# Kernel tuning notes

Measured on AMD Instinct MI355X. Metric: run time of the kernel, lower is better.

Reference implementation:

```python
import jax, jax.numpy as jnp
import numpy as np

D = 2048      # input_dim
E = 64        # num_experts
TOPK = 8
N = 16384     # tokens


def setup_inputs() -> dict:
    key = jax.random.key(0)
    k_x, k_w1, k_b1, k_w2, k_b2 = jax.random.split(key, 5)
    s1 = 1.0 / np.sqrt(D)
    return {
        "x": jax.random.normal(k_x, (N, D), dtype=jnp.float32),
        "W1": jax.random.uniform(k_w1, (D, D), minval=-s1, maxval=s1, dtype=jnp.float32),
        "b1": jax.random.uniform(k_b1, (D,), minval=-s1, maxval=s1, dtype=jnp.float32),
        "W2": jax.random.uniform(k_w2, (D, E), minval=-s1, maxval=s1, dtype=jnp.float32),
        "b2": jax.random.uniform(k_b2, (E,), minval=-s1, maxval=s1, dtype=jnp.float32),
    }


def reference(x, W1, b1, W2, b2):
    # gate MLP: Linear -> GELU (exact, erf-based as torch nn.GELU default) -> Linear
    h = jax.nn.gelu(x @ W1 + b1, approximate=False)
    logits = h @ W2 + b2                              # [N, E]
    # eval mode: no noise added
    top_vals, top_idx = jax.lax.top_k(logits, TOPK)   # [N, K]
    top_w = jax.nn.softmax(top_vals, axis=-1)         # softmax over selected logits
    rows = jnp.arange(logits.shape[0])[:, None]       # [N, 1]
    routing_weights = jnp.zeros_like(logits).at[rows, top_idx].set(top_w)
    # load balance loss
    probs = jax.nn.softmax(logits, axis=-1)
    freq = (routing_weights > 0).astype(logits.dtype).mean(axis=0)   # [E]
    avg_prob = probs.mean(axis=0)                                    # [E]
    load_balance_loss = E * jnp.sum(freq * avg_prob)
    return routing_weights, top_idx, load_balance_loss
```

## Files before the change

### kernel.cpp

```cpp
#include <hip/hip_runtime.h>
#include <math.h>
#include <stdint.h>

#define N_TOK 16384
#define DIM   2048
#define NEXP  64
#define TOPK  8

#define BM 128
#define BN 128
#define BKE 32

typedef _Float16 half8 __attribute__((ext_vector_type(8)));
typedef _Float16 half4 __attribute__((ext_vector_type(4)));
typedef float    f32x4 __attribute__((ext_vector_type(4)));

#define GLOBAL_AS __attribute__((address_space(1)))
#define LDS_AS    __attribute__((address_space(3)))

#define LO_SCALE     4096.0f
#define INV_LO_SCALE (1.0f / 4096.0f)

__device__ inline uint32_t pack_split(float v) {
    _Float16 hi = (_Float16)v;
    float r = (v - (float)hi) * LO_SCALE;
    _Float16 lo = (_Float16)r;
    return (uint32_t)__builtin_bit_cast(uint16_t, hi) |
           ((uint32_t)__builtin_bit_cast(uint16_t, lo) << 16);
}

__device__ inline _Float16 split_hi(float v) { return (_Float16)v; }
__device__ inline _Float16 split_lo(float v) {
    _Float16 hi = (_Float16)v;
    return (_Float16)((v - (float)hi) * LO_SCALE);
}

union U4H8 { uint32_t u[4]; half8 h; };

__device__ inline void load_frag(const uint32_t* base, int row, int quad,
                                 half8& hi, half8& lo) {
    const int sw = row & 7;
    const uint4 q0 = *(const uint4*)(base + row * 32 + (((quad * 2)     ^ sw) << 2));
    const uint4 q1 = *(const uint4*)(base + row * 32 + (((quad * 2 + 1) ^ sw) << 2));
    uint32_t u[8] = {q0.x, q0.y, q0.z, q0.w, q1.x, q1.y, q1.z, q1.w};
    U4H8 H, L;
    #pragma unroll
    for (int j = 0; j < 4; j++) {
        H.u[j] = (u[2 * j] & 0xffffu) | (u[2 * j + 1] << 16);
        L.u[j] = (u[2 * j] >> 16)     | (u[2 * j + 1] & 0xffff0000u);
    }
    hi = H.h; lo = L.h;
}

__device__ inline void load_frag2(const _Float16* base, int row, int quad,
                                  half8& hi, half8& lo) {
    const int sw = row & 7;
    hi = *(const half8*)(base + row * 64 + ((quad       ^ sw) << 3));
    lo = *(const half8*)(base + row * 64 + (((quad + 4) ^ sw) << 3));
}

__global__ __launch_bounds__(256) void convert_x_split(
    const float* __restrict__ x, _Float16* __restrict__ xhi,
    _Float16* __restrict__ xlo)
{
    size_t i = ((size_t)blockIdx.x * 256 + threadIdx.x) * 4;
    float4 v = *(const float4*)(x + i);
    half4 h, l;
    h.x = split_hi(v.x); l.x = split_lo(v.x);
    h.y = split_hi(v.y); l.y = split_lo(v.y);
    h.z = split_hi(v.z); l.z = split_lo(v.z);
    h.w = split_hi(v.w); l.w = split_lo(v.w);
    *(half4*)(xhi + i) = h;
    *(half4*)(xlo + i) = l;
}

__global__ __launch_bounds__(256) void convert_w1t_split(
    const float* __restrict__ W1, _Float16* __restrict__ w1hi,
    _Float16* __restrict__ w1lo)
{
    __shared__ float s[32][33];
    const int k0 = blockIdx.y * 32, n0 = blockIdx.x * 32;
    const int tr = threadIdx.x & 31, tc = threadIdx.x >> 5;
    #pragma unroll
    for (int r = 0; r < 4; r++) {
        int row = tc + r * 8;
        s[row][tr] = W1[(size_t)(k0 + row) * DIM + n0 + tr];
    }
    __syncthreads();
    #pragma unroll
    for (int r = 0; r < 4; r++) {
        int row = tc + r * 8;
        float v = s[tr][row];
        w1hi[(size_t)(n0 + row) * DIM + k0 + tr] = split_hi(v);
        w1lo[(size_t)(n0 + row) * DIM + k0 + tr] = split_lo(v);
    }
}

__global__ __launch_bounds__(256) void convert_w2t(const float* __restrict__ W2,
                                                   uint32_t* __restrict__ W2Tp) {
    int i = blockIdx.x * 256 + threadIdx.x;
    int e = i >> 11, n = i & 2047;
    W2Tp[i] = pack_split(W2[(size_t)n * NEXP + e]);
}

__global__ __launch_bounds__(256) void convert_x_inplace(float* __restrict__ x) {
    size_t i = ((size_t)blockIdx.x * 256 + threadIdx.x) * 4;
    float4 v = *(const float4*)(x + i);
    uint4 p;
    p.x = pack_split(v.x); p.y = pack_split(v.y);
    p.z = pack_split(v.z); p.w = pack_split(v.w);
    *(uint4*)(x + i) = p;
}

__global__ __launch_bounds__(256) void convert_w1t_packed(
    const float* __restrict__ W1, uint32_t* __restrict__ W1Tp)
{
    __shared__ float s[32][33];
    const int k0 = blockIdx.y * 32, n0 = blockIdx.x * 32;
    const int tr = threadIdx.x & 31, tc = threadIdx.x >> 5;
    #pragma unroll
    for (int r = 0; r < 4; r++) {
        int row = tc + r * 8;
        s[row][tr] = W1[(size_t)(k0 + row) * DIM + n0 + tr];
    }
    __syncthreads();
    #pragma unroll
    for (int r = 0; r < 4; r++) {
        int row = tc + r * 8;
        W1Tp[(size_t)(n0 + row) * DIM + k0 + tr] = pack_split(s[tr][row]);
    }
}

__global__ __launch_bounds__(256, 2) void gemm_fused_v2(
    const _Float16* __restrict__ xhi, const _Float16* __restrict__ xlo,
    const _Float16* __restrict__ w1hi, const _Float16* __restrict__ w1lo,
    const float* __restrict__ b1, const uint32_t* __restrict__ W2Tp,
    float* __restrict__ Lp)
{
    __shared__ uint32_t smem[16384];
    _Float16* As = (_Float16*)smem;
    _Float16* Bs = (_Float16*)(smem + 4096);

    const int t    = threadIdx.x;
    const int wid  = t >> 6;
    const int lane = t & 63;
    const int quad = lane >> 4;
    const int l16  = lane & 15;

    const int lin = blockIdx.x;
    const int grp = lin >> 7;
    const int rem = lin & 127;
    const int m0 = (grp * 8 + (rem & 7)) * BM;
    const int n0 = (rem >> 3) * BN;

    const _Float16* gA[4];
    const _Float16* gB[4];
    #pragma unroll
    for (int r = 0; r < 4; r++) {
        int s_lin = r * 256 + t;
        int row = s_lin >> 3;
        int c   = (s_lin & 7) ^ (row & 7);
        gA[r] = (c < 4) ? xhi  + (size_t)(m0 + row) * DIM + c * 8
                        : xlo  + (size_t)(m0 + row) * DIM + (c - 4) * 8;
        gB[r] = (c < 4) ? w1hi + (size_t)(n0 + row) * DIM + c * 8
                        : w1lo + (size_t)(n0 + row) * DIM + (c - 4) * 8;
    }

    f32x4 am[4][4], ac[4][4];
    #pragma unroll
    for (int i = 0; i < 4; i++)
        #pragma unroll
        for (int j = 0; j < 4; j++) { am[i][j] = (f32x4)0.0f; ac[i][j] = (f32x4)0.0f; }

    const int wm = (wid & 1) * 64;
    const int wn = (wid >> 1) * 64;

    for (int k0 = 0; k0 < DIM; k0 += BKE) {
        #pragma unroll
        for (int r = 0; r < 4; r++) {
            const int wslot = (r * 256 + wid * 64) << 2;
            __builtin_amdgcn_global_load_lds((const GLOBAL_AS uint32_t*)gA[r],
                                             (LDS_AS uint32_t*)(smem + wslot), 16, 0, 0);
            __builtin_amdgcn_global_load_lds((const GLOBAL_AS uint32_t*)gB[r],
                                             (LDS_AS uint32_t*)(smem + 4096 + wslot), 16, 0, 0);
            gA[r] += BKE; gB[r] += BKE;
        }
        __syncthreads();

        half8 ah[4], al[4], bh[4], bl[4];
        #pragma unroll
        for (int mt = 0; mt < 4; mt++)
            load_frag2(As, wm + mt * 16 + l16, quad, ah[mt], al[mt]);
        #pragma unroll
        for (int nt = 0; nt < 4; nt++)
            load_frag2(Bs, wn + nt * 16 + l16, quad, bh[nt], bl[nt]);

        #pragma unroll
        for (int mt = 0; mt < 4; mt++)
            #pragma unroll
            for (int nt = 0; nt < 4; nt++) {
                am[mt][nt] = __builtin_amdgcn_mfma_f32_16x16x32_f16(ah[mt], bh[nt], am[mt][nt], 0, 0, 0);
                ac[mt][nt] = __builtin_amdgcn_mfma_f32_16x16x32_f16(ah[mt], bl[nt], ac[mt][nt], 0, 0, 0);
                ac[mt][nt] = __builtin_amdgcn_mfma_f32_16x16x32_f16(al[mt], bh[nt], ac[mt][nt], 0, 0, 0);
            }
        __syncthreads();
    }

    uint32_t* Hs = smem;
    #pragma unroll
    for (int mt = 0; mt < 4; mt++)
        #pragma unroll
        for (int nt = 0; nt < 4; nt++) {
            const int coln = wn + nt * 16 + l16;
            const float b1v = b1[n0 + coln];
            #pragma unroll
            for (int r = 0; r < 4; r++) {
                float h = am[mt][nt][r] + ac[mt][nt][r] * INV_LO_SCALE + b1v;
                h = 0.5f * h * (1.0f + erff(h * 0.70710678118654752440f));
                const int rowm = wm + mt * 16 + quad * 4 + r;
                const int word = rowm * 128 + ((((coln >> 2) ^ (rowm & 7)) << 2) | (coln & 3));
                Hs[word] = pack_split(h);
            }
        }
    __syncthreads();

    f32x4 a2m[2][4], a2c[2][4];
    #pragma unroll
    for (int i = 0; i < 2; i++)
        #pragma unroll
        for (int j = 0; j < 4; j++) { a2m[i][j] = (f32x4)0.0f; a2c[i][j] = (f32x4)0.0f; }

    #pragma unroll
    for (int ks = 0; ks < 4; ks++) {
        half8 a2h[2], a2l[2];
        #pragma unroll
        for (int mt2 = 0; mt2 < 2; mt2++) {
            const int row = wid * 32 + mt2 * 16 + l16;
            const int sw  = row & 7;
            const int cb  = ks * 8 + quad * 2;
            const uint4 q0 = *(const uint4*)(Hs + row * 128 + ((cb ^ sw) << 2));
            const uint4 q1 = *(const uint4*)(Hs + row * 128 + (((cb + 1) ^ sw) << 2));
            uint32_t u[8] = {q0.x, q0.y, q0.z, q0.w, q1.x, q1.y, q1.z, q1.w};
            U4H8 H, L;
            #pragma unroll
            for (int j = 0; j < 4; j++) {
                H.u[j] = (u[2 * j] & 0xffffu) | (u[2 * j + 1] << 16);
                L.u[j] = (u[2 * j] >> 16)     | (u[2 * j + 1] & 0xffff0000u);
            }
            a2h[mt2] = H.h; a2l[mt2] = L.h;
        }
        #pragma unroll
        for (int et = 0; et < 4; et++) {
            const int e = et * 16 + l16;
            const uint32_t* wp = W2Tp + (size_t)e * DIM + n0 + ks * 32 + quad * 8;
            const uint4 q0 = *(const uint4*)wp;
            const uint4 q1 = *(const uint4*)(wp + 4);
            uint32_t u[8] = {q0.x, q0.y, q0.z, q0.w, q1.x, q1.y, q1.z, q1.w};
            U4H8 H, L;
            #pragma unroll
            for (int j = 0; j < 4; j++) {
                H.u[j] = (u[2 * j] & 0xffffu) | (u[2 * j + 1] << 16);
                L.u[j] = (u[2 * j] >> 16)     | (u[2 * j + 1] & 0xffff0000u);
            }
            #pragma unroll
            for (int mt2 = 0; mt2 < 2; mt2++) {
                a2m[mt2][et] = __builtin_amdgcn_mfma_f32_16x16x32_f16(a2h[mt2], H.h, a2m[mt2][et], 0, 0, 0);
                a2c[mt2][et] = __builtin_amdgcn_mfma_f32_16x16x32_f16(a2h[mt2], L.h, a2c[mt2][et], 0, 0, 0);
                a2c[mt2][et] = __builtin_amdgcn_mfma_f32_16x16x32_f16(a2l[mt2], H.h, a2c[mt2][et], 0, 0, 0);
            }
        }
    }

    #pragma unroll
    for (int mt2 = 0; mt2 < 2; mt2++)
        #pragma unroll
        for (int et = 0; et < 4; et++)
            #pragma unroll
            for (int r = 0; r < 4; r++) {
                const float lg = a2m[mt2][et][r] + a2c[mt2][et][r] * INV_LO_SCALE;
                const int rowm = m0 + wid * 32 + mt2 * 16 + quad * 4 + r;
                const int e = et * 16 + l16;
                atomicAdd(&Lp[(size_t)rowm * NEXP + e], lg);
            }
}

__global__ __launch_bounds__(256, 2) void gemm_fused(
    const uint32_t* __restrict__ xp, const uint32_t* __restrict__ W1Tp,
    const float* __restrict__ b1, const uint32_t* __restrict__ W2Tp,
    float* __restrict__ Lp)
{
    __shared__ uint32_t smem[16384];
    uint32_t* Ap = smem;
    uint32_t* Bp = smem + 4096;

    const int t    = threadIdx.x;
    const int wid  = t >> 6;
    const int lane = t & 63;
    const int quad = lane >> 4;
    const int l16  = lane & 15;

    const int lin = blockIdx.x;
    const int grp = lin >> 7;
    const int rem = lin & 127;
    const int m0 = (grp * 8 + (rem & 7)) * BM;
    const int n0 = (rem >> 3) * BN;

    const uint32_t* gA[4];
    const uint32_t* gB[4];
    #pragma unroll
    for (int r = 0; r < 4; r++) {
        int s = r * 256 + t;
        int row = s >> 3;
        int c   = s & 7;
        int co  = (c ^ (row & 7)) << 2;
        gA[r] = xp   + (size_t)(m0 + row) * DIM + co;
        gB[r] = W1Tp + (size_t)(n0 + row) * DIM + co;
    }

    f32x4 am[4][4], ac[4][4];
    #pragma unroll
    for (int i = 0; i < 4; i++)
        #pragma unroll
        for (int j = 0; j < 4; j++) { am[i][j] = (f32x4)0.0f; ac[i][j] = (f32x4)0.0f; }

    const int wm = (wid & 1) * 64;
    const int wn = (wid >> 1) * 64;

    for (int k0 = 0; k0 < DIM; k0 += BKE) {
        #pragma unroll
        for (int r = 0; r < 4; r++) {
            const int wslot = (r * 256 + wid * 64) << 2;
            __builtin_amdgcn_global_load_lds((const GLOBAL_AS uint32_t*)gA[r],
                                             (LDS_AS uint32_t*)(Ap + wslot), 16, 0, 0);
            __builtin_amdgcn_global_load_lds((const GLOBAL_AS uint32_t*)gB[r],
                                             (LDS_AS uint32_t*)(Bp + wslot), 16, 0, 0);
            gA[r] += BKE; gB[r] += BKE;
        }
        __syncthreads();

        half8 ah[4], al[4], bh[4], bl[4];
        #pragma unroll
        for (int mt = 0; mt < 4; mt++)
            load_frag(Ap, wm + mt * 16 + l16, quad, ah[mt], al[mt]);
        #pragma unroll
        for (int nt = 0; nt < 4; nt++)
            load_frag(Bp, wn + nt * 16 + l16, quad, bh[nt], bl[nt]);

        #pragma unroll
        for (int mt = 0; mt < 4; mt++)
            #pragma unroll
            for (int nt = 0; nt < 4; nt++) {
                am[mt][nt] = __builtin_amdgcn_mfma_f32_16x16x32_f16(ah[mt], bh[nt], am[mt][nt], 0, 0, 0);
                ac[mt][nt] = __builtin_amdgcn_mfma_f32_16x16x32_f16(ah[mt], bl[nt], ac[mt][nt], 0, 0, 0);
                ac[mt][nt] = __builtin_amdgcn_mfma_f32_16x16x32_f16(al[mt], bh[nt], ac[mt][nt], 0, 0, 0);
            }
        __syncthreads();
    }

    uint32_t* Hs = smem;
    #pragma unroll
    for (int mt = 0; mt < 4; mt++)
        #pragma unroll
        for (int nt = 0; nt < 4; nt++) {
            const int coln = wn + nt * 16 + l16;
            const float b1v = b1[n0 + coln];
            #pragma unroll
            for (int r = 0; r < 4; r++) {
                float h = am[mt][nt][r] + ac[mt][nt][r] * INV_LO_SCALE + b1v;
                h = 0.5f * h * (1.0f + erff(h * 0.70710678118654752440f));
                const int rowm = wm + mt * 16 + quad * 4 + r;
                const int word = rowm * 128 + ((((coln >> 2) ^ (rowm & 7)) << 2) | (coln & 3));
                Hs[word] = pack_split(h);
            }
        }
    __syncthreads();

    f32x4 a2m[2][4], a2c[2][4];
    #pragma unroll
    for (int i = 0; i < 2; i++)
        #pragma unroll
        for (int j = 0; j < 4; j++) { a2m[i][j] = (f32x4)0.0f; a2c[i][j] = (f32x4)0.0f; }

    #pragma unroll
    for (int ks = 0; ks < 4; ks++) {
        half8 a2h[2], a2l[2];
        #pragma unroll
        for (int mt2 = 0; mt2 < 2; mt2++) {
            const int row = wid * 32 + mt2 * 16 + l16;
            const int sw  = row & 7;
            const int cb  = ks * 8 + quad * 2;
            const uint4 q0 = *(const uint4*)(Hs + row * 128 + ((cb ^ sw) << 2));
            const uint4 q1 = *(const uint4*)(Hs + row * 128 + (((cb + 1) ^ sw) << 2));
            uint32_t u[8] = {q0.x, q0.y, q0.z, q0.w, q1.x, q1.y, q1.z, q1.w};
            U4H8 H, L;
            #pragma unroll
            for (int j = 0; j < 4; j++) {
                H.u[j] = (u[2 * j] & 0xffffu) | (u[2 * j + 1] << 16);
                L.u[j] = (u[2 * j] >> 16)     | (u[2 * j + 1] & 0xffff0000u);
            }
            a2h[mt2] = H.h; a2l[mt2] = L.h;
        }
        #pragma unroll
        for (int et = 0; et < 4; et++) {
            const int e = et * 16 + l16;
            const uint32_t* wp = W2Tp + (size_t)e * DIM + n0 + ks * 32 + quad * 8;
            const uint4 q0 = *(const uint4*)wp;
            const uint4 q1 = *(const uint4*)(wp + 4);
            uint32_t u[8] = {q0.x, q0.y, q0.z, q0.w, q1.x, q1.y, q1.z, q1.w};
            U4H8 H, L;
            #pragma unroll
            for (int j = 0; j < 4; j++) {
                H.u[j] = (u[2 * j] & 0xffffu) | (u[2 * j + 1] << 16);
                L.u[j] = (u[2 * j] >> 16)     | (u[2 * j + 1] & 0xffff0000u);
            }
            #pragma unroll
            for (int mt2 = 0; mt2 < 2; mt2++) {
                a2m[mt2][et] = __builtin_amdgcn_mfma_f32_16x16x32_f16(a2h[mt2], H.h, a2m[mt2][et], 0, 0, 0);
                a2c[mt2][et] = __builtin_amdgcn_mfma_f32_16x16x32_f16(a2h[mt2], L.h, a2c[mt2][et], 0, 0, 0);
                a2c[mt2][et] = __builtin_amdgcn_mfma_f32_16x16x32_f16(a2l[mt2], H.h, a2c[mt2][et], 0, 0, 0);
            }
        }
    }

    #pragma unroll
    for (int mt2 = 0; mt2 < 2; mt2++)
        #pragma unroll
        for (int et = 0; et < 4; et++)
            #pragma unroll
            for (int r = 0; r < 4; r++) {
                const float lg = a2m[mt2][et][r] + a2c[mt2][et][r] * INV_LO_SCALE;
                const int rowm = m0 + wid * 32 + mt2 * 16 + quad * 4 + r;
                const int e = et * 16 + l16;
                atomicAdd(&Lp[(size_t)rowm * NEXP + e], lg);
            }
}

__global__ __launch_bounds__(256) void router_topk_v2(
    const float* __restrict__ Lp, const float* __restrict__ b2,
    float* __restrict__ out_rw, float* __restrict__ out_idx,
    float* __restrict__ gP, float* __restrict__ gI)
{
    __shared__ float sP[NEXP];
    __shared__ float sI[NEXP];
    const int t = threadIdx.x;
    if (t < NEXP) { sP[t] = 0.f; sI[t] = 0.f; }
    __syncthreads();

    const int lane = t & 63;
    const int wv   = t >> 6;
    const float b2v = b2[lane];

    float accP = 0.f, accSel = 0.f;

    for (int i = 0; i < 16; i++) {
        const int tok = blockIdx.x * 64 + i * 4 + wv;
        float logit = Lp[(size_t)tok * NEXP + lane] + b2v;

        float mx = logit;
        #pragma unroll
        for (int off = 32; off >= 1; off >>= 1) mx = fmaxf(mx, __shfl_xor(mx, off));
        float p = expf(logit - mx);
        float ps = p;
        #pragma unroll
        for (int off = 32; off >= 1; off >>= 1) ps += __shfl_xor(ps, off);
        accP += p / ps;

        float cur = logit;
        float tv[TOPK]; int tix[TOPK];
        for (int k = 0; k < TOPK; k++) {
            float v = cur; int idx = lane;
            #pragma unroll
            for (int off = 32; off >= 1; off >>= 1) {
                float ov = __shfl_xor(v, off);
                int   oi = __shfl_xor(idx, off);
                if (ov > v || (ov == v && oi < idx)) { v = ov; idx = oi; }
            }
            tv[k] = v; tix[k] = idx;
            if (lane == idx) cur = -INFINITY;
        }

        float ev[TOPK], s = 0.f;
        #pragma unroll
        for (int k = 0; k < TOPK; k++) { ev[k] = expf(tv[k] - tv[0]); s += ev[k]; }
        float w = 0.f;
        #pragma unroll
        for (int k = 0; k < TOPK; k++)
            if (tix[k] == lane) { w = ev[k] / s; accSel += 1.f; }

        out_rw[(size_t)tok * NEXP + lane] = w;
        if (lane < TOPK) out_idx[(size_t)tok * TOPK + lane] = (float)tix[lane];
    }

    atomicAdd(&sP[lane], accP);
    atomicAdd(&sI[lane], accSel);
    __syncthreads();
    if (t < NEXP) { atomicAdd(&gP[t], sP[t]); atomicAdd(&gI[t], sI[t]); }
}

__global__ void loss_kernel(const float* __restrict__ gP,
                            const float* __restrict__ gI,
                            float* __restrict__ out_loss)
{
    const int lane = threadIdx.x;
    const float inv = 1.0f / (float)N_TOK;
    float v = (gI[lane] * inv) * (gP[lane] * inv);
    #pragma unroll
    for (int off = 32; off >= 1; off >>= 1) v += __shfl_xor(v, off);
    if (lane == 0) out_loss[0] = (float)NEXP * v;
}

extern "C" void kernel_launch(void* const* d_in, const int* in_sizes, int n_in,
                              void* d_out, int out_size, void* d_ws, size_t ws_size,
                              hipStream_t stream) {
    const float* x  = (const float*)d_in[0];
    const float* W1 = (const float*)d_in[1];
    const float* b1 = (const float*)d_in[2];
    const float* W2 = (const float*)d_in[3];
    const float* b2 = (const float*)d_in[4];

    float* out_rw   = (float*)d_out;
    float* out_idx  = out_rw + (size_t)N_TOK * NEXP;
    float* out_loss = out_idx + (size_t)N_TOK * TOPK;

    const size_t SZ_X   = (size_t)N_TOK * DIM * 2;
    const size_t SZ_W1  = (size_t)DIM * DIM * 2;
    const size_t OFF_XHI   = 0;
    const size_t OFF_XLO   = OFF_XHI + SZ_X;
    const size_t OFF_W1HI  = OFF_XLO + SZ_X;
    const size_t OFF_W1LO  = OFF_W1HI + SZ_W1;
    const size_t OFF_W2T   = OFF_W1LO + SZ_W1;
    const size_t OFF_LP    = OFF_W2T + (size_t)DIM * NEXP * 4;
    const size_t OFF_G     = OFF_LP + (size_t)N_TOK * NEXP * 4;
    const size_t needed_v2 = OFF_G + 2 * NEXP * 4;

    const size_t P_W1T = 0;
    const size_t P_W2T = (size_t)16 << 20;
    const size_t P_LP  = (size_t)17 << 20;
    const size_t P_G   = P_LP + (size_t)N_TOK * NEXP * 4;
    const size_t needed_p = P_G + 2 * NEXP * 4;

    if (ws_size >= needed_v2) {
        _Float16* xhi  = (_Float16*)((char*)d_ws + OFF_XHI);
        _Float16* xlo  = (_Float16*)((char*)d_ws + OFF_XLO);
        _Float16* w1hi = (_Float16*)((char*)d_ws + OFF_W1HI);
        _Float16* w1lo = (_Float16*)((char*)d_ws + OFF_W1LO);
        uint32_t* W2Tp = (uint32_t*)((char*)d_ws + OFF_W2T);
        float* Lp = (float*)((char*)d_ws + OFF_LP);
        float* gP = (float*)((char*)d_ws + OFF_G);
        float* gI = gP + NEXP;

        (void)hipMemsetAsync((char*)d_ws + OFF_LP, 0,
                             (size_t)N_TOK * NEXP * 4 + 2 * NEXP * 4, stream);
        convert_x_split  <<<(N_TOK * DIM) / (256 * 4), 256, 0, stream>>>(x, xhi, xlo);
        convert_w1t_split<<<dim3(DIM / 32, DIM / 32), 256, 0, stream>>>(W1, w1hi, w1lo);
        convert_w2t      <<<(NEXP * DIM) / 256, 256, 0, stream>>>(W2, W2Tp);
        gemm_fused_v2<<<(N_TOK / BM) * (DIM / BN), 256, 0, stream>>>(
            xhi, xlo, w1hi, w1lo, b1, W2Tp, Lp);
        router_topk_v2<<<N_TOK / 64, 256, 0, stream>>>(Lp, b2, out_rw, out_idx, gP, gI);
        loss_kernel<<<1, 64, 0, stream>>>(gP, gI, out_loss);
    } else if (ws_size >= needed_p) {
        uint32_t* W1Tp = (uint32_t*)((char*)d_ws + P_W1T);
        uint32_t* W2Tp = (uint32_t*)((char*)d_ws + P_W2T);
        float* Lp = (float*)((char*)d_ws + P_LP);
        float* gP = (float*)((char*)d_ws + P_G);
        float* gI = gP + NEXP;

        (void)hipMemsetAsync((char*)d_ws + P_LP, 0,
                             (size_t)N_TOK * NEXP * 4 + 2 * NEXP * 4, stream);
        convert_x_inplace<<<(N_TOK * DIM) / (256 * 4), 256, 0, stream>>>((float*)d_in[0]);
        convert_w1t_packed<<<dim3(DIM / 32, DIM / 32), 256, 0, stream>>>(W1, W1Tp);
        convert_w2t<<<(NEXP * DIM) / 256, 256, 0, stream>>>(W2, W2Tp);
        gemm_fused<<<(N_TOK / BM) * (DIM / BN), 256, 0, stream>>>(
            (const uint32_t*)d_in[0], W1Tp, b1, W2Tp, Lp);
        router_topk_v2<<<N_TOK / 64, 256, 0, stream>>>(Lp, b2, out_rw, out_idx, gP, gI);
        loss_kernel<<<1, 64, 0, stream>>>(gP, gI, out_loss);
    }
}
```

Measured before the change: 771.7 us.

## Double-buffer LDS tiles in fused GEMM and widen x split conversion

```diff
diff --git a/kernel.cpp b/kernel.cpp
--- a/kernel.cpp
+++ b/kernel.cpp
@@ -63,15 +63,15 @@
     const float* __restrict__ x, _Float16* __restrict__ xhi,
     _Float16* __restrict__ xlo)
 {
-    size_t i = ((size_t)blockIdx.x * 256 + threadIdx.x) * 4;
-    float4 v = *(const float4*)(x + i);
-    half4 h, l;
-    h.x = split_hi(v.x); l.x = split_lo(v.x);
-    h.y = split_hi(v.y); l.y = split_lo(v.y);
-    h.z = split_hi(v.z); l.z = split_lo(v.z);
-    h.w = split_hi(v.w); l.w = split_lo(v.w);
-    *(half4*)(xhi + i) = h;
-    *(half4*)(xlo + i) = l;
+    size_t i = ((size_t)blockIdx.x * 256 + threadIdx.x) * 8;
+    float4 v0 = *(const float4*)(x + i);
+    float4 v1 = *(const float4*)(x + i + 4);
+    const float vv[8] = {v0.x, v0.y, v0.z, v0.w, v1.x, v1.y, v1.z, v1.w};
+    half8 h, l;
+    #pragma unroll
+    for (int j = 0; j < 8; j++) { h[j] = split_hi(vv[j]); l[j] = split_lo(vv[j]); }
+    *(half8*)(xhi + i) = h;
+    *(half8*)(xlo + i) = l;
 }
 
 __global__ __launch_bounds__(256) void convert_w1t_split(
@@ -131,6 +131,47 @@
     }
 }
 
+
+#define KSTEP(ASrc_, BSrc_, ASt_, BSt_, DOSTAGE_)                               \
+    {                                                                           \
+        if (DOSTAGE_) {                                                         \
+            _Pragma("unroll")                                                   \
+            for (int r = 0; r < 4; r++) {                                       \
+                const int wslot = (r * 256 + wid * 64) << 2;                    \
+                __builtin_amdgcn_global_load_lds(                               \
+                    (const GLOBAL_AS uint32_t*)gA[r],                           \
+                    (LDS_AS uint32_t*)((ASt_) + wslot), 16, 0, 0);              \
+                __builtin_amdgcn_global_load_lds(                               \
+                    (const GLOBAL_AS uint32_t*)gB[r],                           \
+                    (LDS_AS uint32_t*)((BSt_) + wslot), 16, 0, 0);              \
+                gA[r] += BKE; gB[r] += BKE;                                     \
+            }                                                                   \
+        }                                                                       \
+        half8 ah[4], al[4], bh[4], bl[4];                                       \
+        _Pragma("unroll")                                                       \
+        for (int mt = 0; mt < 4; mt++)                                          \
+            load_frag2((const _Float16*)(ASrc_), wm + mt * 16 + l16, quad,      \
+                       ah[mt], al[mt]);                                         \
+        _Pragma("unroll")                                                       \
+        for (int nt = 0; nt < 4; nt++)                                          \
+            load_frag2((const _Float16*)(BSrc_), wn + nt * 16 + l16, quad,      \
+                       bh[nt], bl[nt]);                                         \
+        __builtin_amdgcn_s_setprio(1);                                          \
+        _Pragma("unroll")                                                       \
+        for (int mt = 0; mt < 4; mt++)                                          \
+            _Pragma("unroll")                                                   \
+            for (int nt = 0; nt < 4; nt++) {                                    \
+                am[mt][nt] = __builtin_amdgcn_mfma_f32_16x16x32_f16(            \
+                    ah[mt], bh[nt], am[mt][nt], 0, 0, 0);                       \
+                ac[mt][nt] = __builtin_amdgcn_mfma_f32_16x16x32_f16(            \
+                    ah[mt], bl[nt], ac[mt][nt], 0, 0, 0);                       \
+                ac[mt][nt] = __builtin_amdgcn_mfma_f32_16x16x32_f16(            \
+                    al[mt], bh[nt], ac[mt][nt], 0, 0, 0);                       \
+            }                                                                   \
+        __builtin_amdgcn_s_setprio(0);                                          \
+        __syncthreads();                                                        \
+    }
+
 __global__ __launch_bounds__(256, 2) void gemm_fused_v2(
     const _Float16* __restrict__ xhi, const _Float16* __restrict__ xlo,
     const _Float16* __restrict__ w1hi, const _Float16* __restrict__ w1lo,
@@ -138,8 +179,10 @@
     float* __restrict__ Lp)
 {
     __shared__ uint32_t smem[16384];
-    _Float16* As = (_Float16*)smem;
-    _Float16* Bs = (_Float16*)(smem + 4096);
+    uint32_t* A0 = smem;
+    uint32_t* B0 = smem + 4096;
+    uint32_t* A1 = smem + 8192;
+    uint32_t* B1 = smem + 12288;
 
     const int t    = threadIdx.x;
     const int wid  = t >> 6;
@@ -175,35 +218,20 @@
     const int wm = (wid & 1) * 64;
     const int wn = (wid >> 1) * 64;
 
-    for (int k0 = 0; k0 < DIM; k0 += BKE) {
-        #pragma unroll
-        for (int r = 0; r < 4; r++) {
-            const int wslot = (r * 256 + wid * 64) << 2;
-            __builtin_amdgcn_global_load_lds((const GLOBAL_AS uint32_t*)gA[r],
-                                             (LDS_AS uint32_t*)(smem + wslot), 16, 0, 0);
-            __builtin_amdgcn_global_load_lds((const GLOBAL_AS uint32_t*)gB[r],
-                                             (LDS_AS uint32_t*)(smem + 4096 + wslot), 16, 0, 0);
-            gA[r] += BKE; gB[r] += BKE;
-        }
-        __syncthreads();
-
-        half8 ah[4], al[4], bh[4], bl[4];
-        #pragma unroll
-        for (int mt = 0; mt < 4; mt++)
-            load_frag2(As, wm + mt * 16 + l16, quad, ah[mt], al[mt]);
-        #pragma unroll
-        for (int nt = 0; nt < 4; nt++)
-            load_frag2(Bs, wn + nt * 16 + l16, quad, bh[nt], bl[nt]);
-
-        #pragma unroll
-        for (int mt = 0; mt < 4; mt++)
-            #pragma unroll
-            for (int nt = 0; nt < 4; nt++) {
-                am[mt][nt] = __builtin_amdgcn_mfma_f32_16x16x32_f16(ah[mt], bh[nt], am[mt][nt], 0, 0, 0);
-                ac[mt][nt] = __builtin_amdgcn_mfma_f32_16x16x32_f16(ah[mt], bl[nt], ac[mt][nt], 0, 0, 0);
-                ac[mt][nt] = __builtin_amdgcn_mfma_f32_16x16x32_f16(al[mt], bh[nt], ac[mt][nt], 0, 0, 0);
-            }
-        __syncthreads();
+    #pragma unroll
+    for (int r = 0; r < 4; r++) {
+        const int wslot = (r * 256 + wid * 64) << 2;
+        __builtin_amdgcn_global_load_lds((const GLOBAL_AS uint32_t*)gA[r],
+                                         (LDS_AS uint32_t*)(A0 + wslot), 16, 0, 0);
+        __builtin_amdgcn_global_load_lds((const GLOBAL_AS uint32_t*)gB[r],
+                                         (LDS_AS uint32_t*)(B0 + wslot), 16, 0, 0);
+        gA[r] += BKE; gB[r] += BKE;
+    }
+    __syncthreads();
+
+    for (int kp = 0; kp < 32; kp++) {
+        KSTEP(A0, B0, A1, B1, true);
+        KSTEP(A1, B1, A0, B0, kp != 31);
     }
 
     uint32_t* Hs = smem;
@@ -551,7 +579,7 @@
 
         (void)hipMemsetAsync((char*)d_ws + OFF_LP, 0,
                              (size_t)N_TOK * NEXP * 4 + 2 * NEXP * 4, stream);
-        convert_x_split  <<<(N_TOK * DIM) / (256 * 4), 256, 0, stream>>>(x, xhi, xlo);
+        convert_x_split  <<<(N_TOK * DIM) / (256 * 8), 256, 0, stream>>>(x, xhi, xlo);
         convert_w1t_split<<<dim3(DIM / 32, DIM / 32), 256, 0, stream>>>(W1, w1hi, w1lo);
         convert_w2t      <<<(NEXP * DIM) / 256, 256, 0, stream>>>(W2, W2Tp);
         gemm_fused_v2<<<(N_TOK / BM) * (DIM / BN), 256, 0, stream>>>(
```

Result: faster. 739.4 us (-4.2%).
